# Kernel optimization log

Measured on AMD Instinct MI355X. Metric: run time of the kernel, lower is better.

Reference implementation:

```python
import jax, jax.numpy as jnp
import numpy as np

N = 8192
IN_F = 512
OUT_F = 512
ALPHA = 0.2
NEG_BIG = -9.0e15


def setup_inputs() -> dict:
    key = jax.random.key(0)
    k1, k2, k3, k4 = jax.random.split(key, 4)
    adjacency = jax.random.randint(k1, (N, N), 0, 2, dtype=jnp.int32)
    features = jax.random.normal(k2, (N, IN_F), dtype=jnp.float32)
    # Linear weight stored as [in, out] (h = x @ W)
    W = jax.random.normal(k3, (IN_F, OUT_F), dtype=jnp.float32) * (1.0 / np.sqrt(IN_F))
    attn = jax.random.normal(k4, (2 * OUT_F, 1), dtype=jnp.float32) * 0.05
    return {"adjacency": adjacency, "features": features, "W": W, "attn": attn}


def reference(adjacency, features, W, attn):
    h = features @ W  # [N, F]
    # Additive decomposition of concat([h_i, h_j]) @ attn:
    # score_ij = a1 . h_i + a2 . h_j  (identical math, no NxNx2F tensor)
    a1 = attn[:OUT_F, 0]  # [F]
    a2 = attn[OUT_F:, 0]  # [F]
    s1 = h @ a1  # [N] contribution of source node i
    s2 = h @ a2  # [N] contribution of target node j
    e = jax.nn.leaky_relu(s1[:, None] + s2[None, :], negative_slope=ALPHA)  # [N, N]
    e = jnp.where(adjacency > 0, e, NEG_BIG)
    attention = jax.nn.softmax(e, axis=1)  # [N, N]
    h_prime = attention @ h  # [N, F]
    return jax.nn.elu(h_prime)
```

## Files before the change

kernel.cpp:

```cpp
#include <hip/hip_runtime.h>
#include <hip/hip_bf16.h>
#include <cstdint>

#define NN 8192
#define F 512
#define LOG2E 1.4426950408889634f

typedef __attribute__((ext_vector_type(8))) short bf16x8;
typedef __attribute__((ext_vector_type(4))) float f32x4;
typedef unsigned int uint32;
typedef unsigned long long u64;
typedef unsigned char uchar;

__device__ __forceinline__ short f2bf(float x){
  __hip_bfloat16 h = __float2bfloat16(x);
  return *reinterpret_cast<short*>(&h);
}

__global__ __launch_bounds__(256) void k_wa(const float* __restrict__ W, const float* __restrict__ attn,
                     float* __restrict__ wa){
  const int lane = threadIdx.x&63, wid = threadIdx.x>>6;
  const int id = blockIdx.x*4 + wid;
  const int b = id>>9, c = id&511;
  const float4* Wr = (const float4*)(W + (size_t)c*F);
  const float4* av = (const float4*)(attn + b*F);
  float s = 0.f;
  #pragma unroll
  for (int h=0;h<2;++h){
    const int k = lane + h*64;
    const float4 wv = Wr[k], a = av[k];
    s += wv.x*a.x + wv.y*a.y + wv.z*a.z + wv.w*a.w;
  }
  for (int off=32;off;off>>=1) s += __shfl_down(s,off);
  if (lane==0) wa[id] = s;
}

__global__ __launch_bounds__(256) void k_tw(const float* __restrict__ W, short* __restrict__ WbT){
  __shared__ short t[64][72];
  const int k0 = blockIdx.x*64, n0 = blockIdx.y*64;
  #pragma unroll
  for (int it=0;it<16;++it){
    const int idx = it*256 + threadIdx.x;
    const int r = idx>>6, c = idx&63;
    t[r][c] = f2bf(W[(size_t)(k0+r)*F + n0 + c]);
  }
  __syncthreads();
  #pragma unroll
  for (int it=0;it<2;++it){
    const int idx = it*256 + threadIdx.x;
    const int n = idx>>3, g = idx&7;
    short v[8];
    #pragma unroll
    for (int e=0;e<8;++e) v[e] = t[g*8+e][n];
    *(uint4*)(WbT + (size_t)(n0+n)*F + k0 + g*8) = *(const uint4*)v;
  }
}

__global__ __launch_bounds__(256) void k_prep(const float* __restrict__ X, const float* __restrict__ wa,
    short* __restrict__ Xb, float2* __restrict__ rowAB, uint32* __restrict__ uwb){
  const int lane = threadIdx.x&63, wid = threadIdx.x>>6;
  const int row = blockIdx.x*4 + wid;
  const float4* X4 = (const float4*)(X + (size_t)row*F);
  const float4* A4 = (const float4*)wa;
  const float4* B4 = (const float4*)(wa + F);
  uint2* Xb4 = (uint2*)(Xb + (size_t)row*F);
  float a1 = 0.f, a2 = 0.f;
  #pragma unroll
  for (int h=0;h<2;++h){
    const int c = lane + h*64;
    const float4 x = X4[c];
    const float4 a = A4[c];
    const float4 b = B4[c];
    a1 += x.x*a.x + x.y*a.y + x.z*a.z + x.w*a.w;
    a2 += x.x*b.x + x.y*b.y + x.z*b.z + x.w*b.w;
    short o[4] = {f2bf(x.x),f2bf(x.y),f2bf(x.z),f2bf(x.w)};
    Xb4[c] = *(const uint2*)o;
  }
  for (int off=32;off;off>>=1){ a1 += __shfl_down(a1,off); a2 += __shfl_down(a2,off); }
  if (lane==0){
    const float s1 = a1*LOG2E, s2 = a2*LOG2E;
    rowAB[row] = make_float2(exp2f(s1), exp2f(0.2f*s1));
    const float u = exp2f(s2), w = exp2f(0.2f*s2);
    uwb[row] = (uint32)(unsigned short)f2bf(u) | ((uint32)(unsigned short)f2bf(w)<<16);
  }
}

__global__ __launch_bounds__(256,2) void k_gemm1(const short* __restrict__ Xb,
    const short* __restrict__ WbT, short* __restrict__ HT){
  __shared__ char smem[33280];
  short* At = (short*)smem;
  short* Bt = (short*)(smem + 16384);
  const int tid=threadIdx.x, lane=tid&63, wid=tid>>6;
  const int m0 = blockIdx.x*128, n0 = blockIdx.y*128;
  f32x4 acc[2][8];
  #pragma unroll
  for (int a=0;a<2;++a)
    #pragma unroll
    for (int b=0;b<8;++b) acc[a][b] = (f32x4){0.f,0.f,0.f,0.f};

  for (int t=0;t<8;++t){
    const int k0 = t*64;
    __syncthreads();
    #pragma unroll
    for (int rnd=0;rnd<4;++rnd){
      const int s = rnd*256 + tid;
      const int n = s>>3, kc = s&7;
      uint4 va = *(const uint4*)(Xb  + (size_t)(m0+n)*F + k0 + kc*8);
      uint4 vb = *(const uint4*)(WbT + (size_t)(n0+n)*F + k0 + kc*8);
      const int off = n*128 + ((kc^(n&7))*16);
      *(uint4*)((char*)At + off) = va;
      *(uint4*)((char*)Bt + off) = vb;
    }
    __syncthreads();
    #pragma unroll
    for (int ks=0;ks<2;++ks){
      const int kc = ks*4 + (lane>>4);
      int r0 = wid*32 + (lane&15);
      int r1 = r0 + 16;
      bf16x8 af0 = *(const bf16x8*)((char*)At + r0*128 + ((kc^(r0&7))*16));
      bf16x8 af1 = *(const bf16x8*)((char*)At + r1*128 + ((kc^(r1&7))*16));
      #pragma unroll
      for (int nf=0;nf<8;++nf){
        const int c = nf*16 + (lane&15);
        bf16x8 bf = *(const bf16x8*)((char*)Bt + c*128 + ((kc^(c&7))*16));
        acc[0][nf] = __builtin_amdgcn_mfma_f32_16x16x32_bf16(af0, bf, acc[0][nf],0,0,0);
        acc[1][nf] = __builtin_amdgcn_mfma_f32_16x16x32_bf16(af1, bf, acc[1][nf],0,0,0);
      }
    }
  }
  __syncthreads();
  short* ct = (short*)smem;
  #pragma unroll
  for (int mf=0;mf<2;++mf)
    #pragma unroll
    for (int nf=0;nf<8;++nf)
      #pragma unroll
      for (int q=0;q<4;++q){
        int r = wid*32 + mf*16 + (lane>>4)*4 + q;
        int c = nf*16 + (lane&15);
        ct[r*130+c] = f2bf(acc[mf][nf][q]);
      }
  __syncthreads();
  {
    const int c = tid>>1, ih0 = (tid&1)*64;
    #pragma unroll
    for (int i8=0;i8<8;++i8){
      short v[8];
      #pragma unroll
      for (int e=0;e<8;++e) v[e] = ct[(ih0+i8*8+e)*130 + c];
      *(uint4*)(HT + (size_t)(n0+c)*NN + m0 + ih0 + i8*8) = *(const uint4*)v;
    }
  }
}

__global__ __launch_bounds__(256,2) void k_pv(const int* __restrict__ adj,
    const short* __restrict__ HT, const uint32* __restrict__ uwb,
    const float2* __restrict__ rowAB, float* __restrict__ Zp,
    float* __restrict__ P0, float* __restrict__ P1,
    float* __restrict__ P2, float* __restrict__ P3, int ksteps, int KS){
  __shared__ short Bt[512*64];
  __shared__ short At[64*64];
  __shared__ uint32 uwl[2048];
  const int tid=threadIdx.x, lane=tid&63, wid=tid>>6;
  int mx, kz;
  if (KS == 4){
    const int id = blockIdx.x;
    kz = (id&7)>>1;
    mx = ((id>>3)<<1) + (id&1);
  } else { kz = 0; mx = blockIdx.x; }
  const int m0 = mx*64;
  const int kz0 = kz*(ksteps*64);
  float* const outs[4] = {P0,P1,P2,P3};
  float* outP = outs[kz];

  {
    const uint4* src = (const uint4*)(uwb + kz0);
    uint4 v0 = src[tid], v1 = src[256+tid];
    ((uint4*)uwl)[tid] = v0; ((uint4*)uwl)[256+tid] = v1;
  }

  const int kcs = (tid&7) ^ ((tid>>3)&7);
  const short* gBa = HT + (size_t)(tid>>3)*NN + kz0 + kcs*8;

  const int ar = tid>>2, aq = tid&3;
  const float2 E = rowAB[m0 + ar];
  const float A0 = E.x, B0c = E.y;
  const int* adjp = adj + (size_t)(m0+ar)*NN + kz0 + aq*8;
  const int aoff0 = ar*128 + (((aq  ) ^ (ar&7))*16);
  const int aoff1 = ar*128 + (((aq+4) ^ (ar&7))*16);

  f32x4 acc[4][8];
  #pragma unroll
  for (int i=0;i<4;++i)
    #pragma unroll
    for (int j=0;j<8;++j) acc[i][j] = (f32x4){0.f,0.f,0.f,0.f};
  float zacc = 0.f;

  uint4 b0,b1,b2,b3,b4,b5,b6,b7;
  int4  aA0,aA1, aB0,aB1;

#define PV_BLOAD_H(h, tt) { \
    const short* g = gBa + (size_t)(h)*256*NN + (size_t)(tt)*64; \
    b0 = *(const uint4*)(g);                   b1 = *(const uint4*)(g + (size_t)1*32*NN); \
    b2 = *(const uint4*)(g + (size_t)2*32*NN); b3 = *(const uint4*)(g + (size_t)3*32*NN); \
    b4 = *(const uint4*)(g + (size_t)4*32*NN); b5 = *(const uint4*)(g + (size_t)5*32*NN); \
    b6 = *(const uint4*)(g + (size_t)6*32*NN); b7 = *(const uint4*)(g + (size_t)7*32*NN); }

#define PV_BWRITE_H(h) { \
    uint4* d = (uint4*)Bt + (h)*2048; \
    d[      tid] = b0; d[ 256+tid] = b1; d[ 512+tid] = b2; d[ 768+tid] = b3; \
    d[1024+tid] = b4; d[1280+tid] = b5; d[1536+tid] = b6; d[1792+tid] = b7; }

#define PV_ALOAD(r0v,r1v,h,tt) { \
    r0v = *(const int4*)(adjp + (size_t)(tt)*64 + (h)*32); \
    r1v = *(const int4*)(adjp + (size_t)(tt)*64 + (h)*32 + 4); }

#define PV_AGEN(aoffv, r0v, r1v, h, tt) { \
    const uint32* uwt = &uwl[(tt)*64 + (h)*32 + aq*8]; \
    const uint4 u0 = *(const uint4*)uwt; \
    const uint4 u1 = *(const uint4*)(uwt+4); \
    const uint32 pk[8] = {u0.x,u0.y,u0.z,u0.w,u1.x,u1.y,u1.z,u1.w}; \
    const int    aa[8] = {r0v.x,r0v.y,r0v.z,r0v.w,r1v.x,r1v.y,r1v.z,r1v.w}; \
    short av[8]; \
    _Pragma("unroll") \
    for (int e=0;e<8;++e){ \
      const float u = __uint_as_float(pk[e]<<16); \
      const float w = __uint_as_float(pk[e]&0xffff0000u); \
      float v = fmaxf(A0*u, B0c*w); \
      v = (aa[e] > 0) ? v : 0.f; \
      zacc += v; \
      av[e] = f2bf(v); } \
    *(uint4*)((char*)At + (aoffv)) = *(const uint4*)av; }

#define PV_MFMA64() { \
    _Pragma("unroll") \
    for (int ks=0;ks<2;++ks){ \
      const int kc = ks*4 + (lane>>4); \
      bf16x8 af[4]; \
      _Pragma("unroll") \
      for (int mf=0;mf<4;++mf){ \
        const int r = mf*16 + (lane&15); \
        af[mf] = *(const bf16x8*)((char*)At + r*128 + ((kc^(r&7))*16)); } \
      _Pragma("unroll") \
      for (int nf=0;nf<8;++nf){ \
        const int c = wid*128 + nf*16 + (lane&15); \
        const bf16x8 bv = *(const bf16x8*)((char*)Bt + c*128 + ((kc^(c&7))*16)); \
        _Pragma("unroll") \
        for (int mf=0;mf<4;++mf) \
          acc[mf][nf] = __builtin_amdgcn_mfma_f32_16x16x32_bf16(af[mf], bv, acc[mf][nf],0,0,0); } } }

  PV_ALOAD(aA0,aA1, 0, 0);
  PV_ALOAD(aB0,aB1, 1, 0);
  PV_BLOAD_H(0, 0);
  __syncthreads();
  PV_BWRITE_H(0);
  PV_AGEN(aoff0, aA0,aA1, 0, 0);
  PV_BLOAD_H(1, 0);
  PV_AGEN(aoff1, aB0,aB1, 1, 0);
  PV_BWRITE_H(1);
  __syncthreads();

  for (int t=0; t<ksteps; ++t){
    if (t+1 < ksteps){
      PV_BLOAD_H(0, t+1);
      PV_ALOAD(aA0,aA1, 0, t+1);
      PV_ALOAD(aB0,aB1, 1, t+1);
    }
    PV_MFMA64();
    __syncthreads();
    if (t+1 < ksteps){
      PV_BWRITE_H(0);
      PV_AGEN(aoff0, aA0,aA1, 0, t+1);
      PV_BLOAD_H(1, t+1);
      PV_AGEN(aoff1, aB0,aB1, 1, t+1);
      PV_BWRITE_H(1);
      __syncthreads();
    }
  }

  zacc += __shfl_xor(zacc, 1);
  zacc += __shfl_xor(zacc, 2);
  if (aq == 0) Zp[(size_t)kz*NN + m0 + ar] = zacc;
  #pragma unroll
  for (int mf=0;mf<4;++mf)
    #pragma unroll
    for (int nf=0;nf<8;++nf){
      const int col = wid*128 + nf*16 + (lane&15);
      #pragma unroll
      for (int qq=0;qq<4;++qq){
        const int row = m0 + mf*16 + (lane>>4)*4 + qq;
        outP[(size_t)row*F + col] = acc[mf][nf][qq];
      }
    }
#undef PV_BLOAD_H
#undef PV_BWRITE_H
#undef PV_ALOAD
#undef PV_AGEN
#undef PV_MFMA64
}

__global__ __launch_bounds__(256) void k_red(const float* __restrict__ P1,
    const float* __restrict__ P2, const float* __restrict__ P3,
    const float* __restrict__ Zp, float* __restrict__ out, int ks){
  const size_t i = ((size_t)blockIdx.x*256 + threadIdx.x)*4;
  const int row = (int)(i >> 9);
  float4 a = *(float4*)(out+i);
  float Z = Zp[row];
  if (ks > 1){
    Z += Zp[NN+row] + Zp[2*NN+row] + Zp[3*NN+row];
    const float4 b1 = *(const float4*)(P1+i);
    const float4 b2 = *(const float4*)(P2+i);
    const float4 b3 = *(const float4*)(P3+i);
    a.x += b1.x+b2.x+b3.x; a.y += b1.y+b2.y+b3.y;
    a.z += b1.z+b2.z+b3.z; a.w += b1.w+b2.w+b3.w;
  }
  const float s = 1.f/Z;
  a.x*=s; a.y*=s; a.z*=s; a.w*=s;
  a.x = (a.x>0.f)?a.x:expm1f(a.x);
  a.y = (a.y>0.f)?a.y:expm1f(a.y);
  a.z = (a.z>0.f)?a.z:expm1f(a.z);
  a.w = (a.w>0.f)?a.w:expm1f(a.w);
  *(float4*)(out+i) = a;
}

extern "C" void kernel_launch(void* const* d_in, const int* in_sizes, int n_in,
                              void* d_out, int out_size, void* d_ws, size_t ws_size,
                              hipStream_t stream) {
  (void)in_sizes; (void)n_in; (void)out_size;
  const int*   adj  = (const int*)d_in[0];
  const float* X    = (const float*)d_in[1];
  const float* W    = (const float*)d_in[2];
  const float* attn = (const float*)d_in[3];
  float* out = (float*)d_out;
  char* ws = (char*)d_ws;
  short*  HT   = (short*)(ws);
  short*  Xb   = (short*)(ws + 8388608);
  short*  WbT  = (short*)(ws + 16777216);
  uint32* uwb  = (uint32*)(ws + 17301504);
  float2* rowAB= (float2*)(ws + 17334272);
  float*  wa   = (float*)(ws + 17399808);
  float*  Zp   = (float*)(ws + 17403904);
  float*  P1   = (float*)(ws + 17534976);
  float*  P2   = (float*)(ws + 34312192);
  float*  P3   = (float*)(ws + 51089408);
  const int KS = (ws_size >= 67866624ull) ? 4 : 1;
  const int ksteps = 128/KS;

  k_wa   <<<dim3(256),    dim3(256), 0, stream>>>(W, attn, wa);
  k_tw   <<<dim3(8,8),    dim3(256), 0, stream>>>(W, WbT);
  k_prep <<<dim3(2048),   dim3(256), 0, stream>>>(X, wa, Xb, rowAB, uwb);
  k_gemm1<<<dim3(64,4),   dim3(256), 0, stream>>>(Xb, WbT, HT);
  k_pv   <<<dim3(128*KS), dim3(256), 0, stream>>>(adj, HT, uwb, rowAB, Zp, out, P1, P2, P3, ksteps, KS);
  k_red  <<<dim3(4096),   dim3(256), 0, stream>>>(P1, P2, P3, Zp, out, KS);
}
```

Baseline: 152.4 us.

## Load B operand directly from global memory and double-buffer A tile

The PV kernel no longer stages the 512x64 H^T tile in shared memory. Each wave reads its MFMA B fragments straight from global memory (relying on L2/cache reuse across blocks), and the attention A tile becomes double-buffered so only one barrier per k-step is needed. This removes the large LDS footprint and its write/read traffic and cuts a sync, but it exposes global-load latency directly inside the MFMA loop with no software prefetch of B. Each B element is also now fetched by every block sharing the same k range, not once per block into LDS.

```diff
diff --git a/kernel.cpp b/kernel.cpp
--- a/kernel.cpp
+++ b/kernel.cpp
@@ -158,8 +158,7 @@
     const float2* __restrict__ rowAB, float* __restrict__ Zp,
     float* __restrict__ P0, float* __restrict__ P1,
     float* __restrict__ P2, float* __restrict__ P3, int ksteps, int KS){
-  __shared__ short Bt[512*64];
-  __shared__ short At[64*64];
+  __shared__ short At2[2][64*64];
   __shared__ uint32 uwl[2048];
   const int tid=threadIdx.x, lane=tid&63, wid=tid>>6;
   int mx, kz;
@@ -179,8 +178,7 @@
     ((uint4*)uwl)[tid] = v0; ((uint4*)uwl)[256+tid] = v1;
   }
 
-  const int kcs = (tid&7) ^ ((tid>>3)&7);
-  const short* gBa = HT + (size_t)(tid>>3)*NN + kz0 + kcs*8;
+  const short* gBm = HT + (size_t)(wid*128 + (lane&15))*NN + kz0 + (lane>>4)*8;
 
   const int ar = tid>>2, aq = tid&3;
   const float2 E = rowAB[m0 + ar];
@@ -196,26 +194,15 @@
     for (int j=0;j<8;++j) acc[i][j] = (f32x4){0.f,0.f,0.f,0.f};
   float zacc = 0.f;
 
-  uint4 b0,b1,b2,b3,b4,b5,b6,b7;
-  int4  aA0,aA1, aB0,aB1;
-
-#define PV_BLOAD_H(h, tt) { \
-    const short* g = gBa + (size_t)(h)*256*NN + (size_t)(tt)*64; \
-    b0 = *(const uint4*)(g);                   b1 = *(const uint4*)(g + (size_t)1*32*NN); \
-    b2 = *(const uint4*)(g + (size_t)2*32*NN); b3 = *(const uint4*)(g + (size_t)3*32*NN); \
-    b4 = *(const uint4*)(g + (size_t)4*32*NN); b5 = *(const uint4*)(g + (size_t)5*32*NN); \
-    b6 = *(const uint4*)(g + (size_t)6*32*NN); b7 = *(const uint4*)(g + (size_t)7*32*NN); }
-
-#define PV_BWRITE_H(h) { \
-    uint4* d = (uint4*)Bt + (h)*2048; \
-    d[      tid] = b0; d[ 256+tid] = b1; d[ 512+tid] = b2; d[ 768+tid] = b3; \
-    d[1024+tid] = b4; d[1280+tid] = b5; d[1536+tid] = b6; d[1792+tid] = b7; }
-
-#define PV_ALOAD(r0v,r1v,h,tt) { \
-    r0v = *(const int4*)(adjp + (size_t)(tt)*64 + (h)*32); \
-    r1v = *(const int4*)(adjp + (size_t)(tt)*64 + (h)*32 + 4); }
-
-#define PV_AGEN(aoffv, r0v, r1v, h, tt) { \
+  int4 aA0,aA1, aB0,aB1;
+
+#define PV_ALOAD(tt) { \
+    aA0 = *(const int4*)(adjp + (size_t)(tt)*64); \
+    aA1 = *(const int4*)(adjp + (size_t)(tt)*64 + 4); \
+    aB0 = *(const int4*)(adjp + (size_t)(tt)*64 + 32); \
+    aB1 = *(const int4*)(adjp + (size_t)(tt)*64 + 36); }
+
+#define PV_AGEN_H(buf, aoffv, r0v, r1v, h, tt) { \
     const uint32* uwt = &uwl[(tt)*64 + (h)*32 + aq*8]; \
     const uint4 u0 = *(const uint4*)uwt; \
     const uint4 u1 = *(const uint4*)(uwt+4); \
@@ -230,9 +217,9 @@
       v = (aa[e] > 0) ? v : 0.f; \
       zacc += v; \
       av[e] = f2bf(v); } \
-    *(uint4*)((char*)At + (aoffv)) = *(const uint4*)av; }
-
-#define PV_MFMA64() { \
+    *(uint4*)((char*)(At2[buf]) + (aoffv)) = *(const uint4*)av; }
+
+#define PV_MFMA64(buf, tt) { \
     _Pragma("unroll") \
     for (int ks=0;ks<2;++ks){ \
       const int kc = ks*4 + (lane>>4); \
@@ -240,42 +227,28 @@
       _Pragma("unroll") \
       for (int mf=0;mf<4;++mf){ \
         const int r = mf*16 + (lane&15); \
-        af[mf] = *(const bf16x8*)((char*)At + r*128 + ((kc^(r&7))*16)); } \
+        af[mf] = *(const bf16x8*)((char*)(At2[buf]) + r*128 + ((kc^(r&7))*16)); } \
       _Pragma("unroll") \
       for (int nf=0;nf<8;++nf){ \
-        const int c = wid*128 + nf*16 + (lane&15); \
-        const bf16x8 bv = *(const bf16x8*)((char*)Bt + c*128 + ((kc^(c&7))*16)); \
+        const bf16x8 bv = *(const bf16x8*)(gBm + (size_t)nf*16*NN + ks*32 + (size_t)(tt)*64); \
         _Pragma("unroll") \
         for (int mf=0;mf<4;++mf) \
           acc[mf][nf] = __builtin_amdgcn_mfma_f32_16x16x32_bf16(af[mf], bv, acc[mf][nf],0,0,0); } } }
 
-  PV_ALOAD(aA0,aA1, 0, 0);
-  PV_ALOAD(aB0,aB1, 1, 0);
-  PV_BLOAD_H(0, 0);
-  __syncthreads();
-  PV_BWRITE_H(0);
-  PV_AGEN(aoff0, aA0,aA1, 0, 0);
-  PV_BLOAD_H(1, 0);
-  PV_AGEN(aoff1, aB0,aB1, 1, 0);
-  PV_BWRITE_H(1);
+  PV_ALOAD(0);
+  __syncthreads();
+  PV_AGEN_H(0, aoff0, aA0,aA1, 0, 0);
+  PV_AGEN_H(0, aoff1, aB0,aB1, 1, 0);
   __syncthreads();
 
   for (int t=0; t<ksteps; ++t){
+    if (t+1 < ksteps) PV_ALOAD(t+1);
+    PV_MFMA64(t&1, t);
     if (t+1 < ksteps){
-      PV_BLOAD_H(0, t+1);
-      PV_ALOAD(aA0,aA1, 0, t+1);
-      PV_ALOAD(aB0,aB1, 1, t+1);
-    }
-    PV_MFMA64();
+      PV_AGEN_H((t+1)&1, aoff0, aA0,aA1, 0, t+1);
+      PV_AGEN_H((t+1)&1, aoff1, aB0,aB1, 1, t+1);
+    }
     __syncthreads();
-    if (t+1 < ksteps){
-      PV_BWRITE_H(0);
-      PV_AGEN(aoff0, aA0,aA1, 0, t+1);
-      PV_BLOAD_H(1, t+1);
-      PV_AGEN(aoff1, aB0,aB1, 1, t+1);
-      PV_BWRITE_H(1);
-      __syncthreads();
-    }
   }
 
   zacc += __shfl_xor(zacc, 1);
@@ -292,10 +265,8 @@
         outP[(size_t)row*F + col] = acc[mf][nf][qq];
       }
     }
-#undef PV_BLOAD_H
-#undef PV_BWRITE_H
 #undef PV_ALOAD
-#undef PV_AGEN
+#undef PV_AGEN_H
 #undef PV_MFMA64
 }
 
```

Measured after the change: 224.4 us. 1.47x slower.
